# Optimization experiments

Hardware: AMD Instinct MI355X
Metric: run time of the kernel (lower is better)

Reference implementation:

```python
import jax, jax.numpy as jnp
import numpy as np
import math

NUM_HEADS = 4

def _mha(x, in_w, in_b, out_w, out_b, key_mask):
    # x: [V, S, B, E] (seq-first per-frame role tokens), key_mask: [V, S] True=valid role
    V, S, B, E = x.shape
    hd = E // NUM_HEADS
    qkv = jnp.einsum('vsbe,fe->vsbf', x, in_w) + in_b  # torch Linear: x @ W.T
    q, k, v = jnp.split(qkv, 3, axis=-1)
    q = q.reshape(V, S, B, NUM_HEADS, hd) * (1.0 / math.sqrt(hd))
    k = k.reshape(V, S, B, NUM_HEADS, hd)
    v = v.reshape(V, S, B, NUM_HEADS, hd)
    scores = jnp.einsum('vsbhd,vtbhd->vbhst', q, k)
    scores = jnp.where(key_mask[:, None, None, None, :], scores, -jnp.inf)
    w = jax.nn.softmax(scores, axis=-1)
    o = jnp.einsum('vbhst,vtbhd->vsbhd', w, v).reshape(V, S, B, E)
    return jnp.einsum('vsbe,fe->vsbf', o, out_w) + out_b

def setup_inputs() -> dict:
    B, D, V, R, H, MR, G, L = 16, 2048, 504, 190, 32, 6, 2000, 3
    rng = np.random.default_rng(0)
    verb_roles = np.full((V, MR), -1, dtype=np.int32)  # ragged frames, -1 padded (pad_v_r)
    for vi in range(V):
        n = int(rng.integers(1, MR + 1))
        verb_roles[vi, :n] = rng.choice(R, size=n, replace=False)
    group_len = rng.integers(G // 4, G + 1, size=R).astype(np.int32)  # |r_n[r]| per role
    key = jax.random.key(0)
    ks = jax.random.split(key, 6)
    f = jnp.float32
    return dict(
        rep=jax.random.normal(ks[0], (B, D), f),
        W_v=jax.random.normal(ks[1], (D, V), f) / math.sqrt(D),
        b_v=jnp.zeros((V,), f),
        W_r=jax.random.normal(ks[2], (D, R * H), f) / math.sqrt(D),
        b_r=jnp.zeros((R * H,), f),
        attn_in_w=jax.random.normal(ks[3], (L, 3 * H, H), f) / math.sqrt(H),
        attn_in_b=jnp.zeros((L, 3 * H), f),
        attn_out_w=jax.random.normal(ks[4], (L, H, H), f) / math.sqrt(H),
        attn_out_b=jnp.zeros((L, H), f),
        W_n=jax.random.normal(ks[5], (R, H, G), f) / math.sqrt(H),
        b_n=jnp.zeros((R, G), f),
        verb_roles=jnp.asarray(verb_roles),
        group_len=jnp.asarray(group_len),
    )

def reference(rep, W_v, b_v, W_r, b_r, attn_in_w, attn_in_b, attn_out_w, attn_out_b,
              W_n, b_n, verb_roles, group_len):
    B = rep.shape[0]
    V, MR = verb_roles.shape
    R, H, G = W_n.shape
    v_potential = rep @ W_v + b_v                     # [B, V]  linear_v
    node = (rep @ W_r + b_r).reshape(B, R, H)         # [B, R, H]  linear_r
    pos_mask = verb_roles >= 0                        # [V, MR] valid-role mask
    ridx = jnp.maximum(verb_roles, 0)                 # safe gather index
    # gather per-frame role reps: [V, MR, B, H] (seq-first like torch MHA)
    x = jnp.transpose(node[:, ridx, :], (1, 2, 0, 3))
    for l in range(attn_in_w.shape[0]):               # 3 self-attention layers
        x = _mha(x, attn_in_w[l], attn_in_b[l], attn_out_w[l], attn_out_b[l], pos_mask)
    # per-role grouped noun logits (linear_n[r]), ragged groups masked to -inf
    logits = jnp.einsum('vsbh,vshg->vsbg', x, W_n[ridx]) + b_n[ridx][:, :, None, :]  # [V,MR,B,G]
    gmask = jnp.arange(G)[None, None, :] < group_len[ridx][:, :, None]               # [V,MR,G]
    ml = jnp.where(gmask[:, :, None, :], logits, -jnp.inf)
    mmax = jnp.max(ml, axis=-1)                       # [V,MR,B] per-role max (log_sum_exp's max)
    maxi = jnp.argmax(ml, axis=-1)                    # local noun index within group
    lse = mmax + jnp.log(jnp.sum(jnp.exp(ml - mmax[..., None]), axis=-1))
    pm = pos_mask[:, :, None]                         # F.pad(..., value=0) on padded roles
    lse = jnp.where(pm, lse, 0.0)
    mmax = jnp.where(pm, mmax, 0.0)
    maxi = jnp.where(pm, maxi, 0)
    vrn_marginal = jnp.transpose(lse, (2, 0, 1))      # [B, V, MR]
    vr_max = jnp.transpose(mmax, (2, 0, 1))
    vr_maxi = jnp.transpose(maxi, (2, 0, 1))
    v_marginal = vrn_marginal.sum(-1) + v_potential   # [B, V]
    m = jnp.max(v_marginal, axis=1)
    norm = m + jnp.log(jnp.sum(jnp.exp(v_marginal - m[:, None]), axis=1))  # [B]
    v_max = vr_max.sum(-1) + v_potential              # max_max prediction scores
    return (v_potential, norm, v_max, vrn_marginal, vr_max, vr_maxi)
```

## Files before the change

kernel.cpp:

```cpp
#include <hip/hip_runtime.h>
#include <math.h>

constexpr int kB = 16;
constexpr int kD = 2048;
constexpr int kV = 504;
constexpr int kR = 190;
constexpr int kH = 32;
constexpr int kMR = 6;
constexpr int kG = 2000;
constexpr int kL = 3;
constexpr int kNH = 4;
constexpr int kHD = 8;
constexpr int kC1 = kV + kR * kH;
constexpr int kNDS = 8;
constexpr int kDCH = kD / kNDS;

constexpr int kQS = 100;

constexpr int kMAXP = 64;
constexpr int kGCH = 500;
constexpr int kGC = 4;

constexpr size_t WS_NODE = 0;
constexpr size_t WS_X    = WS_NODE + (size_t)kB*kR*kH;
constexpr size_t WS_REST = WS_X + (size_t)kV*kMR*kB*kH;
constexpr size_t WS_PART = WS_REST;
constexpr size_t WS_PM   = WS_REST;
constexpr size_t WS_PS   = WS_PM + (size_t)kV*kMR*kB*kGC;
constexpr size_t WS_PI   = WS_PS + (size_t)kV*kMR*kB*kGC;
constexpr size_t WS_CNT  = WS_PI + (size_t)kV*kMR*kB*kGC;
constexpr size_t WS_PAIR = WS_CNT + kR;

constexpr size_t O_VPOT = 0;
constexpr size_t O_NORM = O_VPOT + (size_t)kB*kV;
constexpr size_t O_VMAX = O_NORM + kB;
constexpr size_t O_VRN  = O_VMAX + (size_t)kB*kV;
constexpr size_t O_VRM  = O_VRN + (size_t)kB*kV*kMR;
constexpr size_t O_VRI  = O_VRM + (size_t)kB*kV*kMR;

__device__ inline float dot4(float4 a, float4 w, float acc) {
  return fmaf(a.x, w.x, fmaf(a.y, w.y, fmaf(a.z, w.z, fmaf(a.w, w.w, acc))));
}

__global__ __launch_bounds__(256) void k1a(const float* __restrict__ rep,
                                           const float* __restrict__ Wv,
                                           const float* __restrict__ Wr,
                                           float* __restrict__ part) {
  __shared__ float rl[kB][kDCH];
  const int tid = threadIdx.x;
  const int col = blockIdx.x * 256 + tid;
  const int d0 = blockIdx.y * kDCH;
  for (int i = tid; i < kB * kDCH; i += 256) {
    int b = i >> 8, dd = i & (kDCH - 1);
    rl[b][dd] = rep[b * kD + d0 + dd];
  }
  __syncthreads();
  if (col >= kC1) return;
  const float* Wp;
  int stride;
  if (col < kV) { Wp = Wv + (size_t)d0 * kV + col; stride = kV; }
  else          { Wp = Wr + (size_t)d0 * (kR*kH) + (col - kV); stride = kR*kH; }
  float acc[kB];
#pragma unroll
  for (int b = 0; b < kB; b++) acc[b] = 0.f;
  for (int dd = 0; dd < kDCH; dd++) {
    float w = Wp[(size_t)dd * stride];
#pragma unroll
    for (int b = 0; b < kB; b++) acc[b] += rl[b][dd] * w;
  }
  float* p = part + (size_t)(blockIdx.y * kB) * kC1 + col;
#pragma unroll
  for (int b = 0; b < kB; b++) p[(size_t)b * kC1] = acc[b];
}

__global__ __launch_bounds__(256) void k1b(const float* __restrict__ part,
                                           const float* __restrict__ bv,
                                           const float* __restrict__ br,
                                           float* __restrict__ out,
                                           float* __restrict__ node) {
  int idx = blockIdx.x * 256 + threadIdx.x;
  if (idx >= kB * kC1) return;
  int b = idx / kC1, col = idx % kC1;
  float s = 0.f;
#pragma unroll
  for (int ds = 0; ds < kNDS; ds++) s += part[(size_t)(ds * kB + b) * kC1 + col];
  if (col < kV) out[O_VPOT + (size_t)b * kV + col] = s + bv[col];
  else          node[(size_t)b * (kR*kH) + (col - kV)] = s + br[col - kV];
}

__global__ __launch_bounds__(256) void k0(const int* __restrict__ verb_roles,
                                          int* __restrict__ cnt,
                                          int* __restrict__ pairs) {
  const int tid = threadIdx.x;
  for (int i = tid; i < kR; i += 256) cnt[i] = 0;
  __syncthreads();
  for (int i = tid; i < kV * kMR; i += 256) {
    int r = verb_roles[i];
    if (r >= 0) {
      int pos = atomicAdd(&cnt[r], 1);
      if (pos < kMAXP) pairs[r * kMAXP + pos] = i;
    }
  }
}

__global__ __launch_bounds__(384) void k2(const float* __restrict__ node,
                                          const int* __restrict__ verb_roles,
                                          const float* __restrict__ in_w,
                                          const float* __restrict__ in_b,
                                          const float* __restrict__ out_w,
                                          const float* __restrict__ out_b,
                                          float* __restrict__ xout) {
  __shared__ float wi[96 * 44];
  __shared__ float wo[32 * 44];
  __shared__ float bi[96];
  __shared__ float bo[32];
  __shared__ float qkv[96 * kQS];
  __shared__ int roles[kMR];
  const int v = blockIdx.x;
  const int tid = threadIdx.x;
  if (tid < kMR) roles[tid] = verb_roles[v * kMR + tid];
  __syncthreads();
  const int rp = tid >> 3, oct = tid & 7;
  const int row0 = 2 * rp, row1 = row0 + 1;
  const int s0 = row0 >> 4, b0 = row0 & 15;
  const int s1 = row1 >> 4, b1 = row1 & 15;
  float4 xr[2][8];
  {
    int r0 = roles[s0] < 0 ? 0 : roles[s0];
    int r1 = roles[s1] < 0 ? 0 : roles[s1];
    const float4* xp0 = (const float4*)(node + (size_t)b0 * (kR*kH) + r0 * kH);
    const float4* xp1 = (const float4*)(node + (size_t)b1 * (kR*kH) + r1 * kH);
#pragma unroll
    for (int j = 0; j < 8; j++) { xr[0][j] = xp0[j]; xr[1][j] = xp1[j]; }
  }
  for (int l = 0; l < kL; l++) {
    for (int i = tid; i < 96 * 32; i += 384) wi[(i >> 5) * 44 + (i & 31)] = in_w[(size_t)l*96*32 + i];
    for (int i = tid; i < 32 * 32; i += 384) wo[(i >> 5) * 44 + (i & 31)] = out_w[(size_t)l*32*32 + i];
    if (tid < 96) bi[tid] = in_b[l*96 + tid];
    else if (tid < 128) bo[tid - 96] = out_b[l*32 + (tid - 96)];
    __syncthreads();
#pragma unroll
    for (int fi = 0; fi < 12; fi++) {
      const int f = oct + 8 * fi;
      const float4* wr = (const float4*)&wi[f * 44];
      float a0 = 0.f, a1 = 0.f, a2 = 0.f, a3 = 0.f;
      float c0 = 0.f, c1 = 0.f, c2 = 0.f, c3 = 0.f;
#pragma unroll
      for (int j = 0; j < 8; j += 4) {
        float4 w0 = wr[j], w1 = wr[j+1], w2 = wr[j+2], w3 = wr[j+3];
        a0 = dot4(xr[0][j],   w0, a0);  c0 = dot4(xr[1][j],   w0, c0);
        a1 = dot4(xr[0][j+1], w1, a1);  c1 = dot4(xr[1][j+1], w1, c1);
        a2 = dot4(xr[0][j+2], w2, a2);  c2 = dot4(xr[1][j+2], w2, c2);
        a3 = dot4(xr[0][j+3], w3, a3);  c3 = dot4(xr[1][j+3], w3, c3);
      }
      const float bf = bi[f];
      qkv[row0 * kQS + f] = ((a0 + a1) + (a2 + a3)) + bf;
      qkv[row1 * kQS + f] = ((c0 + c1) + (c2 + c3)) + bf;
    }
    __syncthreads();
    {
      const int us = tid >> 6, uh = (tid >> 4) & 3, ub = tid & 15;
      const int base = (us * 16 + ub) * kQS + uh * 8;
      float q[8];
#pragma unroll
      for (int d = 0; d < 8; d++) q[d] = qkv[base + d] * 0.35355339059327373f;
      float sc[kMR];
      float mx = -INFINITY;
#pragma unroll
      for (int t = 0; t < kMR; t++) {
        const int kb = (t * 16 + ub) * kQS + 32 + uh * 8;
        float a = 0.f;
#pragma unroll
        for (int d = 0; d < 8; d++) a = fmaf(q[d], qkv[kb + d], a);
        sc[t] = a;
        if (roles[t] >= 0 && a > mx) mx = a;
      }
      float sum = 0.f;
#pragma unroll
      for (int t = 0; t < kMR; t++) {
        float e = (roles[t] >= 0) ? __expf(sc[t] - mx) : 0.f;
        sc[t] = e; sum += e;
      }
      const float inv = 1.f / sum;
      float o[8];
#pragma unroll
      for (int d = 0; d < 8; d++) o[d] = 0.f;
#pragma unroll
      for (int t = 0; t < kMR; t++) {
        const float w = sc[t] * inv;
        const int vb = (t * 16 + ub) * kQS + 64 + uh * 8;
#pragma unroll
        for (int d = 0; d < 8; d++) o[d] = fmaf(w, qkv[vb + d], o[d]);
      }
#pragma unroll
      for (int d = 0; d < 8; d++) qkv[base + d] = o[d];
    }
    __syncthreads();
    {
      const float4* o0 = (const float4*)&qkv[row0 * kQS];
      const float4* o1 = (const float4*)&qkv[row1 * kQS];
#pragma unroll
      for (int j = 0; j < 8; j++) { xr[0][j] = o0[j]; xr[1][j] = o1[j]; }
    }
    float acc0[4], acc1[4];
#pragma unroll
    for (int ci = 0; ci < 4; ci++) {
      const int c2 = oct + 8 * ci;
      const float4* wr = (const float4*)&wo[c2 * 44];
      float a0 = 0.f, a1 = 0.f, a2 = 0.f, a3 = 0.f;
      float d0 = 0.f, d1 = 0.f, d2 = 0.f, d3 = 0.f;
#pragma unroll
      for (int j = 0; j < 8; j += 4) {
        float4 w0 = wr[j], w1 = wr[j+1], w2 = wr[j+2], w3 = wr[j+3];
        a0 = dot4(xr[0][j],   w0, a0);  d0 = dot4(xr[1][j],   w0, d0);
        a1 = dot4(xr[0][j+1], w1, a1);  d1 = dot4(xr[1][j+1], w1, d1);
        a2 = dot4(xr[0][j+2], w2, a2);  d2 = dot4(xr[1][j+2], w2, d2);
        a3 = dot4(xr[0][j+3], w3, a3);  d3 = dot4(xr[1][j+3], w3, d3);
      }
      const float bc = bo[c2];
      acc0[ci] = ((a0 + a1) + (a2 + a3)) + bc;
      acc1[ci] = ((d0 + d1) + (d2 + d3)) + bc;
    }
#pragma unroll
    for (int ci = 0; ci < 4; ci++) {
      qkv[row0 * kQS + 32 + oct + 8 * ci] = acc0[ci];
      qkv[row1 * kQS + 32 + oct + 8 * ci] = acc1[ci];
    }
    __syncthreads();
    if (l < kL - 1) {
      const float4* n0 = (const float4*)&qkv[row0 * kQS + 32];
      const float4* n1 = (const float4*)&qkv[row1 * kQS + 32];
#pragma unroll
      for (int j = 0; j < 8; j++) { xr[0][j] = n0[j]; xr[1][j] = n1[j]; }
      __syncthreads();
    }
  }
  for (int i = tid; i < 96 * 32; i += 384) {
    const int row = i >> 5, h = i & 31;
    xout[(size_t)v * (96 * 32) + i] = qkv[row * kQS + 32 + h];
  }
}

__global__ __launch_bounds__(256) void k3a(const float* __restrict__ xw,
                                           const int* __restrict__ cnt,
                                           const int* __restrict__ pairs,
                                           const int* __restrict__ group_len,
                                           const float* __restrict__ Wn,
                                           const float* __restrict__ bn,
                                           float* __restrict__ PM,
                                           float* __restrict__ PS,
                                           float* __restrict__ PI) {
  __shared__ float Wl[kGCH * 36];
  __shared__ float Bl[kGCH];
  __shared__ float mbM[4][8][kB], mbS[4][8][kB], mbI[4][8][kB];
  const int r = blockIdx.x, gc = blockIdx.y;
  const int glen = group_len[r];
  const int g0 = gc * kGCH;
  if (g0 >= glen) return;
  int c = cnt[r]; if (c > kMAXP) c = kMAXP;
  if (c == 0) return;
  const int gn = (kGCH < glen - g0) ? kGCH : (glen - g0);
  const int tid = threadIdx.x;
  const float* W = Wn + (size_t)r * kH * kG + g0;
  const float* bias = bn + (size_t)r * kG + g0;
  for (int g = tid; g < gn; g += 256) {
#pragma unroll
    for (int h = 0; h < kH; h++) Wl[g * 36 + h] = W[(size_t)h * kG + g];
    Bl[g] = bias[g];
  }
  __syncthreads();
  const int wave = tid >> 6, lane = tid & 63;
  const int b = lane & 15, slot = lane >> 4;
  int gw0 = wave * 125, gw1 = gw0 + 125;
  gw0 = (gw0 < gn) ? gw0 : gn;
  gw1 = (gw1 < gn) ? gw1 : gn;
  const int nq = (c + 7) >> 3;
  for (int q = 0; q < nq; q++) {
    const int p0 = 8 * q + 2 * slot, p1 = p0 + 1;
    const bool v0 = p0 < c, v1 = p1 < c;
    const int pr0 = pairs[r * kMAXP + (v0 ? p0 : 0)];
    const int pr1 = pairs[r * kMAXP + (v1 ? p1 : 0)];
    float4 x0[8], x1[8];
    {
      const float4* xp0 = (const float4*)(xw + ((size_t)pr0 * kB + b) * kH);
      const float4* xp1 = (const float4*)(xw + ((size_t)pr1 * kB + b) * kH);
#pragma unroll
      for (int j = 0; j < 8; j++) { x0[j] = xp0[j]; x1[j] = xp1[j]; }
    }
    float m0 = -INFINITY, s0 = 0.f, m1 = -INFINITY, s1 = 0.f;
    int i0 = 0, i1 = 0;
#pragma unroll 2
    for (int g = gw0; g < gw1; g++) {
      const float4* wr = (const float4*)&Wl[g * 36];
      const float bg = Bl[g];
      float a0 = 0.f, a1 = 0.f, a2 = 0.f, a3 = 0.f;
      float c0 = 0.f, c1 = 0.f, c2 = 0.f, c3 = 0.f;
#pragma unroll
      for (int j = 0; j < 8; j += 4) {
        float4 w0 = wr[j], w1 = wr[j+1], w2 = wr[j+2], w3 = wr[j+3];
        a0 = dot4(x0[j],   w0, a0);  c0 = dot4(x1[j],   w0, c0);
        a1 = dot4(x0[j+1], w1, a1);  c1 = dot4(x1[j+1], w1, c1);
        a2 = dot4(x0[j+2], w2, a2);  c2 = dot4(x1[j+2], w2, c2);
        a3 = dot4(x0[j+3], w3, a3);  c3 = dot4(x1[j+3], w3, c3);
      }
      const float acc0 = ((a0 + a1) + (a2 + a3)) + bg;
      const float acc1 = ((c0 + c1) + (c2 + c3)) + bg;
      {
        float d = acc0 - m0; bool gt = d > 0.f;
        float e = __expf(gt ? -d : d);
        s0 = gt ? fmaf(s0, e, 1.f) : s0 + e;
        i0 = gt ? g0 + g : i0;  m0 = gt ? acc0 : m0;
      }
      {
        float d = acc1 - m1; bool gt = d > 0.f;
        float e = __expf(gt ? -d : d);
        s1 = gt ? fmaf(s1, e, 1.f) : s1 + e;
        i1 = gt ? g0 + g : i1;  m1 = gt ? acc1 : m1;
      }
    }
    mbM[wave][2*slot][b]   = v0 ? m0 : -INFINITY;
    mbS[wave][2*slot][b]   = s0;
    mbI[wave][2*slot][b]   = (float)i0;
    mbM[wave][2*slot+1][b] = v1 ? m1 : -INFINITY;
    mbS[wave][2*slot+1][b] = s1;
    mbI[wave][2*slot+1][b] = (float)i1;
    __syncthreads();
    if (tid < 128) {
      const int pl = tid >> 4, bb = tid & 15;
      const int pg = 8 * q + pl;
      if (pg < c) {
        float M = -INFINITY, S = 0.f; int I = 0;
#pragma unroll
        for (int w = 0; w < 4; w++) {
          float om = mbM[w][pl][bb];
          float os = mbS[w][pl][bb];
          int oi = (int)mbI[w][pl][bb];
          if (om != -INFINITY) {
            if (M == -INFINITY)      { M = om; S = os; I = oi; }
            else if (om > M)         { S = S * __expf(M - om) + os; M = om; I = oi; }
            else if (om < M)         { S = S + os * __expf(om - M); }
            else                     { S += os; I = (oi < I) ? oi : I; }
          }
        }
        const int pr2 = pairs[r * kMAXP + pg];
        size_t o = ((size_t)pr2 * kB + bb) * kGC + gc;
        PM[o] = M; PS[o] = S; PI[o] = (float)I;
      }
    }
    __syncthreads();
  }
}

__device__ inline void lse_merge(float& m, float& s, int& i, float om, float os, int oi) {
  if (om == -INFINITY) return;
  if (m == -INFINITY) { m = om; s = os; i = oi; return; }
  if (om > m)       { s = s * __expf(m - om) + os; m = om; i = oi; }
  else if (om < m)  { s = s + os * __expf(om - m); }
  else              { s += os; i = (oi < i) ? oi : i; }
}

__global__ __launch_bounds__(256) void k3b(const int* __restrict__ verb_roles,
                                           const int* __restrict__ group_len,
                                           const float* __restrict__ PM,
                                           const float* __restrict__ PS,
                                           const float* __restrict__ PI,
                                           float* __restrict__ out) {
  const int idx = blockIdx.x * 256 + threadIdx.x;
  if (idx >= kV * kMR * kB) return;
  const int pr = idx >> 4;
  const int b = idx & 15;
  const int v = pr / kMR, s = pr % kMR;
  const size_t o = ((size_t)b * kV + v) * kMR + s;
  const int r = verb_roles[pr];
  if (r < 0) {
    out[O_VRN + o] = 0.f; out[O_VRM + o] = 0.f; out[O_VRI + o] = 0.f;
    return;
  }
  const int glen = group_len[r];
  const int ngc = (glen + kGCH - 1) / kGCH;
  float M = -INFINITY, S = 0.f; int I = 0;
  for (int gc = 0; gc < ngc; gc++) {
    size_t po = ((size_t)pr * kB + b) * kGC + gc;
    lse_merge(M, S, I, PM[po], PS[po], (int)PI[po]);
  }
  out[O_VRN + o] = M + logf(S);
  out[O_VRM + o] = M;
  out[O_VRI + o] = (float)I;
}

__global__ __launch_bounds__(256) void k4(float* __restrict__ out) {
  const int b = blockIdx.x;
  const int tid = threadIdx.x;
  float M = -INFINITY, S = 0.f;
  for (int v = tid; v < kV; v += 256) {
    float sm = 0.f, sx = 0.f;
#pragma unroll
    for (int s = 0; s < kMR; s++) {
      size_t o = ((size_t)b * kV + v) * kMR + s;
      sm += out[O_VRN + o];
      sx += out[O_VRM + o];
    }
    float vp = out[O_VPOT + (size_t)b * kV + v];
    float vm = sm + vp;
    out[O_VMAX + (size_t)b * kV + v] = sx + vp;
    float nm = fmaxf(M, vm);
    S = S * __expf(M - nm) + __expf(vm - nm);
    M = nm;
  }
#pragma unroll
  for (int off = 1; off < 64; off <<= 1) {
    float om = __shfl_xor(M, off);
    float os = __shfl_xor(S, off);
    if (om != -INFINITY) {
      if (M == -INFINITY) { M = om; S = os; }
      else if (om > M) { S = S * __expf(M - om) + os; M = om; }
      else { S += os * __expf(om - M); }
    }
  }
  __shared__ float rm2[4], rs2[4];
  const int wave = tid >> 6, lane = tid & 63;
  if (lane == 0) { rm2[wave] = M; rs2[wave] = S; }
  __syncthreads();
  if (tid == 0) {
    float Mm = rm2[0], Ss = rs2[0];
    for (int w = 1; w < 4; w++) {
      float om = rm2[w], os = rs2[w];
      if (om > Mm) { Ss = Ss * __expf(Mm - om) + os; Mm = om; }
      else { Ss += os * __expf(om - Mm); }
    }
    out[O_NORM + b] = Mm + logf(Ss);
  }
}

extern "C" void kernel_launch(void* const* d_in, const int* in_sizes, int n_in,
                              void* d_out, int out_size, void* d_ws, size_t ws_size,
                              hipStream_t stream) {
  const float* rep = (const float*)d_in[0];
  const float* Wv  = (const float*)d_in[1];
  const float* bv  = (const float*)d_in[2];
  const float* Wr  = (const float*)d_in[3];
  const float* br  = (const float*)d_in[4];
  const float* aiw = (const float*)d_in[5];
  const float* aib = (const float*)d_in[6];
  const float* aow = (const float*)d_in[7];
  const float* aob = (const float*)d_in[8];
  const float* Wn  = (const float*)d_in[9];
  const float* bnn = (const float*)d_in[10];
  const int* vrl   = (const int*)d_in[11];
  const int* gl    = (const int*)d_in[12];
  float* out = (float*)d_out;
  float* ws  = (float*)d_ws;
  int* icnt  = (int*)(ws + WS_CNT);
  int* ipair = (int*)(ws + WS_PAIR);

  k1a<<<dim3((kC1 + 255) / 256, kNDS), 256, 0, stream>>>(rep, Wv, Wr, ws + WS_PART);
  k1b<<<(kB * kC1 + 255) / 256, 256, 0, stream>>>(ws + WS_PART, bv, br, out, ws + WS_NODE);
  k0<<<1, 256, 0, stream>>>(vrl, icnt, ipair);
  k2<<<kV, 384, 0, stream>>>(ws + WS_NODE, vrl, aiw, aib, aow, aob, ws + WS_X);
  k3a<<<dim3(kR, kGC), 256, 0, stream>>>(ws + WS_X, icnt, ipair, gl, Wn, bnn,
                                         ws + WS_PM, ws + WS_PS, ws + WS_PI);
  k3b<<<(kV * kMR * kB + 255) / 256, 256, 0, stream>>>(vrl, gl, ws + WS_PM, ws + WS_PS,
                                                       ws + WS_PI, out);
  k4<<<kB, 256, 0, stream>>>(out);
}
```

Before: 227.6 us.

## Pre-transpose noun weights to g-major layout and read them directly from global

Adds a kernel that transposes W_n into a [R, G, H] workspace buffer so each noun's 32 weights are contiguous, and a new k3a variant that streams those weights straight from global/L2 as float4 instead of staging a transposed 500x32 tile in LDS. The aim is to drop the strided LDS staging pass and its large shared-memory footprint, which raises occupancy for k3a. In exchange it adds a full extra read and write of W_n every call (about 49 MB) and depends on the workspace being large enough, falling back to the old path otherwise.

New measurement: 366.1 us. 60.9% more time.

```diff
diff --git a/kernel.cpp b/kernel.cpp
--- a/kernel.cpp
+++ b/kernel.cpp
@@ -30,6 +30,7 @@
 constexpr size_t WS_PI   = WS_PS + (size_t)kV*kMR*kB*kGC;
 constexpr size_t WS_CNT  = WS_PI + (size_t)kV*kMR*kB*kGC;
 constexpr size_t WS_PAIR = WS_CNT + kR;
+constexpr size_t WS_WT   = WS_REST + 842752;
 
 constexpr size_t O_VPOT = 0;
 constexpr size_t O_NORM = O_VPOT + (size_t)kB*kV;
@@ -101,6 +102,26 @@
       if (pos < kMAXP) pairs[r * kMAXP + pos] = i;
     }
   }
+}
+
+__global__ __launch_bounds__(256) void k3t(const float* __restrict__ Wn,
+                                           const int* __restrict__ group_len,
+                                           float* __restrict__ WT) {
+  const int r = blockIdx.x, y = blockIdx.y;
+  const int glen = group_len[r];
+  const int ga = y * 250;
+  if (ga >= glen) return;
+  const int gb = (ga + 250 < glen) ? ga + 250 : glen;
+  const int g = ga + threadIdx.x;
+  if (g >= gb) return;
+  const float* src = Wn + (size_t)r * kH * kG + g;
+  float tmp[kH];
+#pragma unroll
+  for (int h = 0; h < kH; h++) tmp[h] = src[(size_t)h * kG];
+  float4* dst = (float4*)(WT + ((size_t)r * kG + g) * kH);
+#pragma unroll
+  for (int j = 0; j < kH / 4; j++)
+    dst[j] = make_float4(tmp[4*j], tmp[4*j+1], tmp[4*j+2], tmp[4*j+3]);
 }
 
 __global__ __launch_bounds__(384) void k2(const float* __restrict__ node,
@@ -241,15 +262,117 @@
   }
 }
 
-__global__ __launch_bounds__(256) void k3a(const float* __restrict__ xw,
-                                           const int* __restrict__ cnt,
-                                           const int* __restrict__ pairs,
-                                           const int* __restrict__ group_len,
-                                           const float* __restrict__ Wn,
-                                           const float* __restrict__ bn,
-                                           float* __restrict__ PM,
-                                           float* __restrict__ PS,
-                                           float* __restrict__ PI) {
+__global__ __launch_bounds__(256) void k3a_dir(const float* __restrict__ xw,
+                                               const int* __restrict__ cnt,
+                                               const int* __restrict__ pairs,
+                                               const int* __restrict__ group_len,
+                                               const float* __restrict__ WT,
+                                               const float* __restrict__ bn,
+                                               float* __restrict__ PM,
+                                               float* __restrict__ PS,
+                                               float* __restrict__ PI) {
+  __shared__ float mbM[4][8][kB], mbS[4][8][kB], mbI[4][8][kB];
+  const int r = blockIdx.x, gc = blockIdx.y;
+  const int glen = group_len[r];
+  const int g0 = gc * kGCH;
+  if (g0 >= glen) return;
+  int c = cnt[r]; if (c > kMAXP) c = kMAXP;
+  if (c == 0) return;
+  const int gn = (kGCH < glen - g0) ? kGCH : (glen - g0);
+  const int tid = threadIdx.x;
+  const float* Wb = WT + ((size_t)r * kG + g0) * kH;
+  const float* bias = bn + (size_t)r * kG + g0;
+  const int wave = tid >> 6, lane = tid & 63;
+  const int b = lane & 15, slot = lane >> 4;
+  int gw0 = wave * 125, gw1 = gw0 + 125;
+  gw0 = (gw0 < gn) ? gw0 : gn;
+  gw1 = (gw1 < gn) ? gw1 : gn;
+  const int nq = (c + 7) >> 3;
+  for (int q = 0; q < nq; q++) {
+    const int p0 = 8 * q + 2 * slot, p1 = p0 + 1;
+    const bool v0 = p0 < c, v1 = p1 < c;
+    const int pr0 = pairs[r * kMAXP + (v0 ? p0 : 0)];
+    const int pr1 = pairs[r * kMAXP + (v1 ? p1 : 0)];
+    float4 x0[8], x1[8];
+    {
+      const float4* xp0 = (const float4*)(xw + ((size_t)pr0 * kB + b) * kH);
+      const float4* xp1 = (const float4*)(xw + ((size_t)pr1 * kB + b) * kH);
+#pragma unroll
+      for (int j = 0; j < 8; j++) { x0[j] = xp0[j]; x1[j] = xp1[j]; }
+    }
+    float m0 = -INFINITY, s0 = 0.f, m1 = -INFINITY, s1 = 0.f;
+    int i0 = 0, i1 = 0;
+#pragma unroll 2
+    for (int g = gw0; g < gw1; g++) {
+      const float4* wr = (const float4*)(Wb + (size_t)g * kH);
+      const float bg = bias[g];
+      float a0 = 0.f, a1 = 0.f, a2 = 0.f, a3 = 0.f;
+      float c0 = 0.f, c1 = 0.f, c2 = 0.f, c3 = 0.f;
+#pragma unroll
+      for (int j = 0; j < 8; j += 4) {
+        float4 w0 = wr[j], w1 = wr[j+1], w2 = wr[j+2], w3 = wr[j+3];
+        a0 = dot4(x0[j],   w0, a0);  c0 = dot4(x1[j],   w0, c0);
+        a1 = dot4(x0[j+1], w1, a1);  c1 = dot4(x1[j+1], w1, c1);
+        a2 = dot4(x0[j+2], w2, a2);  c2 = dot4(x1[j+2], w2, c2);
+        a3 = dot4(x0[j+3], w3, a3);  c3 = dot4(x1[j+3], w3, c3);
+      }
+      const float acc0 = ((a0 + a1) + (a2 + a3)) + bg;
+      const float acc1 = ((c0 + c1) + (c2 + c3)) + bg;
+      {
+        float d = acc0 - m0; bool gt = d > 0.f;
+        float e = __expf(gt ? -d : d);
+        s0 = gt ? fmaf(s0, e, 1.f) : s0 + e;
+        i0 = gt ? g0 + g : i0;  m0 = gt ? acc0 : m0;
+      }
+      {
+        float d = acc1 - m1; bool gt = d > 0.f;
+        float e = __expf(gt ? -d : d);
+        s1 = gt ? fmaf(s1, e, 1.f) : s1 + e;
+        i1 = gt ? g0 + g : i1;  m1 = gt ? acc1 : m1;
+      }
+    }
+    mbM[wave][2*slot][b]   = v0 ? m0 : -INFINITY;
+    mbS[wave][2*slot][b]   = s0;
+    mbI[wave][2*slot][b]   = (float)i0;
+    mbM[wave][2*slot+1][b] = v1 ? m1 : -INFINITY;
+    mbS[wave][2*slot+1][b] = s1;
+    mbI[wave][2*slot+1][b] = (float)i1;
+    __syncthreads();
+    if (tid < 128) {
+      const int pl = tid >> 4, bb = tid & 15;
+      const int pg = 8 * q + pl;
+      if (pg < c) {
+        float M = -INFINITY, S = 0.f; int I = 0;
+#pragma unroll
+        for (int w = 0; w < 4; w++) {
+          float om = mbM[w][pl][bb];
+          float os = mbS[w][pl][bb];
+          int oi = (int)mbI[w][pl][bb];
+          if (om != -INFINITY) {
+            if (M == -INFINITY)      { M = om; S = os; I = oi; }
+            else if (om > M)         { S = S * __expf(M - om) + os; M = om; I = oi; }
+            else if (om < M)         { S = S + os * __expf(om - M); }
+            else                     { S += os; I = (oi < I) ? oi : I; }
+          }
+        }
+        const int pr2 = pairs[r * kMAXP + pg];
+        size_t o = ((size_t)pr2 * kB + bb) * kGC + gc;
+        PM[o] = M; PS[o] = S; PI[o] = (float)I;
+      }
+    }
+    __syncthreads();
+  }
+}
+
+__global__ __launch_bounds__(256) void k3a_lds(const float* __restrict__ xw,
+                                               const int* __restrict__ cnt,
+                                               const int* __restrict__ pairs,
+                                               const int* __restrict__ group_len,
+                                               const float* __restrict__ Wn,
+                                               const float* __restrict__ bn,
+                                               float* __restrict__ PM,
+                                               float* __restrict__ PS,
+                                               float* __restrict__ PI) {
   __shared__ float Wl[kGCH * 36];
   __shared__ float Bl[kGCH];
   __shared__ float mbM[4][8][kB], mbS[4][8][kB], mbI[4][8][kB];
@@ -452,13 +575,21 @@
   float* ws  = (float*)d_ws;
   int* icnt  = (int*)(ws + WS_CNT);
   int* ipair = (int*)(ws + WS_PAIR);
+  float* wt  = ws + WS_WT;
+
+  const bool fast = ws_size >= (WS_WT + (size_t)kR * kG * kH) * sizeof(float);
 
   k1a<<<dim3((kC1 + 255) / 256, kNDS), 256, 0, stream>>>(rep, Wv, Wr, ws + WS_PART);
   k1b<<<(kB * kC1 + 255) / 256, 256, 0, stream>>>(ws + WS_PART, bv, br, out, ws + WS_NODE);
   k0<<<1, 256, 0, stream>>>(vrl, icnt, ipair);
+  if (fast) k3t<<<dim3(kR, 8), 256, 0, stream>>>(Wn, gl, wt);
   k2<<<kV, 384, 0, stream>>>(ws + WS_NODE, vrl, aiw, aib, aow, aob, ws + WS_X);
-  k3a<<<dim3(kR, kGC), 256, 0, stream>>>(ws + WS_X, icnt, ipair, gl, Wn, bnn,
-                                         ws + WS_PM, ws + WS_PS, ws + WS_PI);
+  if (fast)
+    k3a_dir<<<dim3(kR, kGC), 256, 0, stream>>>(ws + WS_X, icnt, ipair, gl, wt, bnn,
+                                               ws + WS_PM, ws + WS_PS, ws + WS_PI);
+  else
+    k3a_lds<<<dim3(kR, kGC), 256, 0, stream>>>(ws + WS_X, icnt, ipair, gl, Wn, bnn,
+                                               ws + WS_PM, ws + WS_PS, ws + WS_PI);
   k3b<<<(kV * kMR * kB + 255) / 256, 256, 0, stream>>>(vrl, gl, ws + WS_PM, ws + WS_PS,
                                                        ws + WS_PI, out);
   k4<<<kB, 256, 0, stream>>>(out);
```
